# Optimization experiments

Measured on AMD Instinct MI355X. Metric: run time of the kernel, lower is better.

## Reference

```python
import jax, jax.numpy as jnp
import numpy as np

N_ATOM, N_FRAG, N_EDGE, N_FEDGE, N_MEM = 131072, 32768, 262144, 65536, 196608
B, H, IN_A, IN_F, IN_E, L, OUT = 4096, 256, 64, 32, 16, 4, 1


def setup_inputs():
    ks = iter(jax.random.split(jax.random.key(0), 96))

    def nrm(shape, s=0.05):
        return jax.random.normal(next(ks), shape, jnp.float32) * s

    def ri(shape, hi):
        return jax.random.randint(next(ks), shape, 0, hi)

    z = lambda *s: jnp.zeros(s, jnp.float32)
    o = lambda *s: jnp.ones(s, jnp.float32)
    return {
        'x': nrm((N_ATOM, IN_A), 1.0),
        'fragments': nrm((N_FRAG, IN_F), 1.0),
        'edge_attr': nrm((N_EDGE, IN_E), 1.0),
        'atom_enc_W': nrm((IN_A, H)), 'atom_enc_b': z(H),
        'frag_enc_W': nrm((IN_F, H)), 'frag_enc_b': z(H),
        'bond_W': nrm((L, IN_E, H)), 'bond_b': z(L, H),
        'gine_eps': z(L),
        'gine_W1': nrm((L, H, 2 * H)), 'gine_b1': z(L, 2 * H),
        'gine_bn_g': o(L, 2 * H), 'gine_bn_b': z(L, 2 * H),
        'gine_W2': nrm((L, 2 * H, H)), 'gine_b2': z(L, H),
        'atom_bn_g': o(L, H), 'atom_bn_b': z(L, H),
        'gin_eps': z(L),
        'gin_W1': nrm((L, H, 2 * H)), 'gin_b1': z(L, 2 * H),
        'gin_bn_g': o(L, 2 * H), 'gin_bn_b': z(L, 2 * H),
        'gin_W2': nrm((L, 2 * H, H)), 'gin_b2': z(L, H),
        'frag_bn_g': o(L, H), 'frag_bn_b': z(L, H),
        'a2f_W': nrm((L, H, H)), 'a2f_b': z(L, H),
        'f2a_W': nrm((L, H, H)), 'f2a_b': z(L, H),
        'fo_W1': nrm((H, H)), 'fo_b1': z(H), 'fo_W2': nrm((H, H)), 'fo_b2': z(H),
        'ao_W1': nrm((H, H)), 'ao_b1': z(H), 'ao_W2': nrm((H, H)), 'ao_b2': z(H),
        'out_W1': nrm((H, H)), 'out_b1': z(H), 'out_W2': nrm((H, OUT)), 'out_b2': z(OUT),
        'edge_index': ri((2, N_EDGE), N_ATOM),
        'frag_edge_index': ri((2, N_FEDGE), N_FRAG),
        'batch': jnp.sort(ri((N_ATOM,), B)),
        'fragments_batch': jnp.sort(ri((N_FRAG,), B)),
        'mem_atom': ri((N_MEM,), N_ATOM),
        'mem_frag': ri((N_MEM,), N_FRAG),
    }


def _bn(x, g, b):
    # training-mode BatchNorm1d over the node dimension
    m = x.mean(0)
    v = jnp.mean((x - m) ** 2, 0)
    return (x - m) * jax.lax.rsqrt(v + 1e-5) * g + b


def _seg_sum(v, i, n):
    return jax.ops.segment_sum(v, i, num_segments=n)


def _seg_mean(v, i, n):
    s = _seg_sum(v, i, n)
    c = _seg_sum(jnp.ones((v.shape[0], 1), v.dtype), i, n)
    return s / jnp.maximum(c, 1.0)


def _forward(x, fragments, edge_attr, atom_enc_W, atom_enc_b, frag_enc_W, frag_enc_b, bond_W, bond_b, gine_eps, gine_W1, gine_b1, gine_bn_g, gine_bn_b, gine_W2, gine_b2, atom_bn_g, atom_bn_b, gin_eps, gin_W1, gin_b1, gin_bn_g, gin_bn_b, gin_W2, gin_b2, frag_bn_g, frag_bn_b, a2f_W, a2f_b, f2a_W, f2a_b, fo_W1, fo_b1, fo_W2, fo_b2, ao_W1, ao_b1, ao_W2, ao_b2, out_W1, out_b1, out_W2, out_b2, edge_index, frag_edge_index, batch, fragments_batch, mem_atom, mem_frag):
    a = x @ atom_enc_W + atom_enc_b            # [N_ATOM, H] atom encoder
    f = fragments @ frag_enc_W + frag_enc_b    # [N_FRAG, H] clique encoder
    src, dst = edge_index[0], edge_index[1]
    fsrc, fdst = frag_edge_index[0], frag_edge_index[1]
    n_atom, n_frag = a.shape[0], f.shape[0]
    for l in range(L):
        # per-layer bond encoder (learned_edge_rep=False)
        e = edge_attr @ bond_W[l] + bond_b[l]
        # GINEConv: sum_j relu(x_j + e_ij) gathered to target i
        agg = _seg_sum(jax.nn.relu(a[src] + e), dst, n_atom)
        h = (1.0 + gine_eps[l]) * a + agg
        h = jax.nn.relu(_bn(h @ gine_W1[l] + gine_b1[l], gine_bn_g[l], gine_bn_b[l]))
        a = jax.nn.relu(_bn(h @ gine_W2[l] + gine_b2[l], atom_bn_g[l], atom_bn_b[l]))
        # fragment GINConv on fragment graph
        fagg = _seg_sum(f[fsrc], fdst, n_frag)
        hf = (1.0 + gin_eps[l]) * f + fagg
        hf = jax.nn.relu(_bn(hf @ gin_W1[l] + gin_b1[l], gin_bn_g[l], gin_bn_b[l]))
        f = jax.nn.relu(_bn(hf @ gin_W2[l] + gin_b2[l], frag_bn_g[l], frag_bn_b[l]))
        # inter message passing over atom-fragment membership edges (mean reduce)
        f = f + _seg_mean(jax.nn.relu(a[mem_atom] @ a2f_W[l] + a2f_b[l]), mem_frag, n_frag)
        a = a + _seg_mean(jax.nn.relu(f[mem_frag] @ f2a_W[l] + f2a_b[l]), mem_atom, n_atom)
    # graph-level readout (mean pooling per molecule)
    fp = _seg_mean(f, fragments_batch, B)
    fp = jax.nn.relu(jax.nn.relu(fp @ fo_W1 + fo_b1) @ fo_W2 + fo_b2)
    ap = _seg_mean(a, batch, B)
    ap = jax.nn.relu(jax.nn.relu(ap @ ao_W1 + ao_b1) @ ao_W2 + ao_b2)
    zz = ap + fp
    return jax.nn.relu(zz @ out_W1 + out_b1) @ out_W2 + out_b2  # [B, OUT]


def reference(x, fragments, edge_attr, atom_enc_W, atom_enc_b, frag_enc_W, frag_enc_b, bond_W, bond_b, gine_eps, gine_W1, gine_b1, gine_bn_g, gine_bn_b, gine_W2, gine_b2, atom_bn_g, atom_bn_b, gin_eps, gin_W1, gin_b1, gin_bn_g, gin_bn_b, gin_W2, gin_b2, frag_bn_g, frag_bn_b, a2f_W, a2f_b, f2a_W, f2a_b, fo_W1, fo_b1, fo_W2, fo_b2, ao_W1, ao_b1, ao_W2, ao_b2, out_W1, out_b1, out_W2, out_b2, edge_index, frag_edge_index, batch, fragments_batch, mem_atom, mem_frag):
    return _forward(x, fragments, edge_attr, atom_enc_W, atom_enc_b, frag_enc_W, frag_enc_b, bond_W, bond_b, gine_eps, gine_W1, gine_b1, gine_bn_g, gine_bn_b, gine_W2, gine_b2, atom_bn_g, atom_bn_b, gin_eps, gin_W1, gin_b1, gin_bn_g, gin_bn_b, gin_W2, gin_b2, frag_bn_g, frag_bn_b, a2f_W, a2f_b, f2a_W, f2a_b, fo_W1, fo_b1, fo_W2, fo_b2, ao_W1, ao_b1, ao_W2, ao_b2, out_W1, out_b1, out_W2, out_b2, edge_index, frag_edge_index, batch, fragments_batch, mem_atom, mem_frag)
```

## Files before the change

kernel.cpp:

```cpp
#include <hip/hip_runtime.h>

#define CDIV(a,b) (((a)+(b)-1)/(b))

static const int N_ATOM = 131072, N_FRAG = 32768, N_EDGE = 262144,
                 N_FEDGE = 65536, N_MEM = 196608, BATCH = 4096, H = 256;
static const int NREP = 16;

typedef unsigned short ushort_t;
typedef _Float16 half8_t __attribute__((ext_vector_type(8)));
typedef float    floatx4 __attribute__((ext_vector_type(4)));

struct PanelsIn  { const ushort_t* p[4]; };
struct PanelsOut { ushort_t* p[4]; };

__device__ __forceinline__ float h2f(ushort_t u) {
    _Float16 h; __builtin_memcpy(&h, &u, 2); return (float)h;
}
__device__ __forceinline__ ushort_t f2h(float f) {
    _Float16 h = (_Float16)f; ushort_t u; __builtin_memcpy(&u, &h, 2); return u;
}

__device__ __forceinline__ void load_lds16(const ushort_t* g, ushort_t* l) {
    __builtin_amdgcn_global_load_lds(
        (const __attribute__((address_space(1))) unsigned int*)g,
        (__attribute__((address_space(3))) unsigned int*)l, 16, 0, 0);
}

__global__ void fill_const(float* p, long n, float v) {
    long t = (long)blockIdx.x * blockDim.x + threadIdx.x;
    long stride = (long)gridDim.x * blockDim.x;
    for (; t < n; t += stride) p[t] = v;
}

__global__ void conv_f2h(const float* __restrict__ in, ushort_t* __restrict__ out, long n)
{
    long t = (long)blockIdx.x * 256 + threadIdx.x;
    long stride = (long)gridDim.x * 256;
    for (long i = t; i < n / 4; i += stride) {
        float4 v = ((const float4*)in)[i];
        ushort4 o; o.x = f2h(v.x); o.y = f2h(v.y); o.z = f2h(v.z); o.w = f2h(v.w);
        ((ushort4*)out)[i] = o;
    }
}

__global__ void prep_w(const float* __restrict__ s0, const float* __restrict__ s1,
                       const float* __restrict__ s2, const float* __restrict__ s3,
                       const float* __restrict__ s4, const float* __restrict__ s5,
                       const float* __restrict__ s6, const float* __restrict__ s7,
                       ushort_t* __restrict__ hi, ushort_t* __restrict__ lo)
{
    long gid = (long)blockIdx.x * 256 + threadIdx.x;
    const float* src; int K, M; long base, loc;
    if      (gid < 524288)  { src=s0; K=256; M=512; base=0;       loc=gid; }
    else if (gid < 1048576) { src=s1; K=512; M=256; base=524288;  loc=gid-524288; }
    else if (gid < 1572864) { src=s2; K=256; M=512; base=1048576; loc=gid-1048576; }
    else if (gid < 2097152) { src=s3; K=512; M=256; base=1572864; loc=gid-1572864; }
    else if (gid < 2359296) { src=s4; K=256; M=256; base=2097152; loc=gid-2097152; }
    else if (gid < 2621440) { src=s5; K=256; M=256; base=2359296; loc=gid-2359296; }
    else if (gid < 2637824) { src=s6; K=64;  M=256; base=2621440; loc=gid-2621440; }
    else if (gid < 2646016) { src=s7; K=32;  M=256; base=2637824; loc=gid-2637824; }
    else return;
    long msz = (long)K * M;
    int  mat = (int)(loc / msz); long rem = loc - (long)mat * msz;
    int  k = (int)(rem / M);     int  n = (int)(rem - (long)k * M);
    float v = src[loc];
    ushort_t hu = f2h(v);
    ushort_t lu = f2h(v - h2f(hu));
    int nl = n & 127, g = (k >> 3) & 3;
    long p = (long)((nl >> 4) * 64 + g * 16 + (nl & 15));
    long dst = base + (long)mat * msz + (long)(k >> 5) * ((long)M << 5)
             + ((long)(n >> 7) << 12) + (p << 3) + (k & 7);
    hi[dst] = hu;
    if (lo) lo[dst] = lu;
}

template<int RELU>
__global__ __launch_bounds__(256)
void mfma_gemm(PanelsIn Ap, int astride, const ushort_t* __restrict__ Wh,
               const ushort_t* __restrict__ Wl, const float* __restrict__ bias,
               PanelsOut Cp, int cstride, const float* __restrict__ Aff,
               float* __restrict__ cstatR, int N, int K, int M)
{
    __shared__ ushort_t Asm[4096];
    __shared__ ushort_t Bhs[4096];
    __shared__ ushort_t Bls[4096];
    __shared__ ushort_t AffS[1024];
    const int tid = threadIdx.x;
    const int brow = blockIdx.y * 128, bcol = blockIdx.x * 128;
    const int wid = tid >> 6, lane = tid & 63;
    const int wm = wid >> 1, wn = wid & 1;
    const int lg = lane >> 4, lr = lane & 15;

    if (Aff) {
        for (int c = tid; c < K; c += 256) {
            AffS[c]       = f2h(Aff[c]);
            AffS[512 + c] = f2h(Aff[K + c]);
        }
        __syncthreads();
    }

    const int mA = lane & 15;
    const int gA = (lane >> 4) & 3;

    floatx4 acc[4][4];
    #pragma unroll
    for (int i = 0; i < 4; ++i)
        #pragma unroll
        for (int j = 0; j < 4; ++j) acc[i][j] = (floatx4){0.f, 0.f, 0.f, 0.f};

    const int nkt = K >> 5;
    for (int kt = 0; kt < nkt; ++kt) {
        if (kt) __syncthreads();
        const ushort_t* pa = Ap.p[kt >> 2];
        const ushort_t* ga = pa + (long)(brow + wid * 16 + mA) * astride
                                + ((kt & 3) << 5) + gA * 8;
        load_lds16(ga, Asm + wid * 512);
        load_lds16(ga + (long)64 * astride, Asm + 2048 + wid * 512);
        const ushort_t* gb = Wh + (size_t)kt * ((size_t)M << 5)
                                + ((size_t)bcol << 5) + (wid * 64 + lane) * 8;
        load_lds16(gb, Bhs + wid * 512);
        load_lds16(gb + 2048, Bhs + 2048 + wid * 512);
        if (Wl) {
            const ushort_t* gl = Wl + (size_t)kt * ((size_t)M << 5)
                                    + ((size_t)bcol << 5) + (wid * 64 + lane) * 8;
            load_lds16(gl, Bls + wid * 512);
            load_lds16(gl + 2048, Bls + 2048 + wid * 512);
        }
        __syncthreads();

        half8_t af[4], bh[4], bl[4];
        #pragma unroll
        for (int i = 0; i < 4; ++i)
            af[i] = *(const half8_t*)(Asm + (((wm * 4 + i) * 64 + lg * 16 + lr) << 3));
        if (Aff) {
            half8_t scv = *(const half8_t*)(AffS + (kt << 5) + lg * 8);
            half8_t sbv = *(const half8_t*)(AffS + 512 + (kt << 5) + lg * 8);
            #pragma unroll
            for (int i = 0; i < 4; ++i) {
                half8_t z = af[i] * scv + sbv;
                #pragma unroll
                for (int e = 0; e < 8; ++e)
                    z[e] = z[e] > (_Float16)0 ? z[e] : (_Float16)0;
                af[i] = z;
            }
        }
        #pragma unroll
        for (int j = 0; j < 4; ++j) {
            bh[j] = *(const half8_t*)(Bhs + (((wn * 4 + j) * 64 + lg * 16 + lr) << 3));
            if (Wl)
                bl[j] = *(const half8_t*)(Bls + (((wn * 4 + j) * 64 + lg * 16 + lr) << 3));
        }
        #pragma unroll
        for (int i = 0; i < 4; ++i)
            #pragma unroll
            for (int j = 0; j < 4; ++j) {
                acc[i][j] = __builtin_amdgcn_mfma_f32_16x16x32_f16(af[i], bh[j], acc[i][j], 0, 0, 0);
                if (Wl)
                    acc[i][j] = __builtin_amdgcn_mfma_f32_16x16x32_f16(af[i], bl[j], acc[i][j], 0, 0, 0);
            }
    }

    ushort_t* cb = Cp.p[blockIdx.x];
    float csl[4], cql[4];
    #pragma unroll
    for (int j = 0; j < 4; ++j) { csl[j] = 0.f; cql[j] = 0.f; }
    #pragma unroll
    for (int j = 0; j < 4; ++j) {
        int lcol = wn * 64 + j * 16 + lr;
        float bia = bias[bcol + lcol];
        #pragma unroll
        for (int i = 0; i < 4; ++i) {
            #pragma unroll
            for (int r = 0; r < 4; ++r) {
                int row = brow + wm * 64 + i * 16 + (lg << 2) + r;
                float v = acc[i][j][r] + bia;
                if (RELU) v = fmaxf(v, 0.f);
                ushort_t uo = f2h(v);
                cb[(long)row * cstride + lcol] = uo;
                if (cstatR) {
                    float vq = h2f(uo);
                    csl[j] += vq; cql[j] = fmaf(vq, vq, cql[j]);
                }
            }
        }
    }
    if (cstatR) {
        __syncthreads();
        float* cs = (float*)Asm;
        float* cq = (float*)Bhs;
        if (tid < 128) { cs[tid] = 0.f; cq[tid] = 0.f; }
        __syncthreads();
        #pragma unroll
        for (int j = 0; j < 4; ++j) {
            int cl = wn * 64 + j * 16 + lr;
            atomicAdd(&cs[cl], csl[j]);
            atomicAdd(&cq[cl], cql[j]);
        }
        __syncthreads();
        if (tid < 128) {
            int rep = blockIdx.y & (NREP - 1);
            atomicAdd(&cstatR[(long)rep * 2 * M + bcol + tid], cs[tid]);
            atomicAdd(&cstatR[(long)rep * 2 * M + M + bcol + tid], cq[tid]);
        }
    }
}

__global__ void finalize_aff(const float* __restrict__ cstatR, int M, float invN,
                             const float* __restrict__ g, const float* __restrict__ b,
                             float* __restrict__ aff)
{
    int c = blockIdx.x * blockDim.x + threadIdx.x;
    if (c >= M) return;
    float s = 0.f, q = 0.f;
    for (int r = 0; r < NREP; ++r) {
        s += cstatR[(long)r * 2 * M + c];
        q += cstatR[(long)r * 2 * M + M + c];
    }
    float m = s * invN, var = q * invN - m * m;
    float sa = rsqrtf(var + 1e-5f) * g[c];
    aff[c] = sa; aff[M + c] = b[c] - m * sa;
}

template<int EB>
__global__ __launch_bounds__(256)
void csr_agg(const ushort_t* __restrict__ in, ushort_t* __restrict__ out,
             const int* __restrict__ offs, const int* __restrict__ elist,
             const int* __restrict__ esrc, const float* __restrict__ eattr,
             const float* __restrict__ Wb, const float* __restrict__ bb,
             const float* __restrict__ eps_p, int n_nodes)
{
    __shared__ float Ws[EB ? 4096 : 1];
    __shared__ float bs[EB ? 256 : 1];
    if (EB) {
        for (int i = threadIdx.x; i < 4096; i += 256) Ws[i] = Wb[i];
        bs[threadIdx.x] = bb[threadIdx.x];
        __syncthreads();
    }
    float epsv = 1.f + eps_p[0];
    int lane = threadIdx.x & 63;
    int gw = (blockIdx.x * 256 + threadIdx.x) >> 6;
    int nw = (gridDim.x * 256) >> 6;
    for (int u = gw; u < n_nodes; u += nw) {
        const ushort_t* own = in + (long)u * 256;
        float acc[4];
        #pragma unroll
        for (int j = 0; j < 4; ++j) acc[j] = epsv * h2f(own[lane + 64 * j]);
        int s = offs[u], e = offs[u + 1];
        for (int i = s; i < e; ++i) {
            int eid = elist[i];
            int sid = esrc[eid];
            const ushort_t* row = in + (long)sid * 256;
            if (EB) {
                float ev[16];
                const float4* ea = (const float4*)(eattr + (long)eid * 16);
                float4 e0 = ea[0], e1 = ea[1], e2 = ea[2], e3 = ea[3];
                ev[0]=e0.x; ev[1]=e0.y; ev[2]=e0.z; ev[3]=e0.w;
                ev[4]=e1.x; ev[5]=e1.y; ev[6]=e1.z; ev[7]=e1.w;
                ev[8]=e2.x; ev[9]=e2.y; ev[10]=e2.z; ev[11]=e2.w;
                ev[12]=e3.x; ev[13]=e3.y; ev[14]=e3.z; ev[15]=e3.w;
                #pragma unroll
                for (int j = 0; j < 4; ++j) {
                    int c = lane + 64 * j;
                    float m = bs[c];
                    #pragma unroll
                    for (int k = 0; k < 16; ++k) m = fmaf(ev[k], Ws[k * 256 + c], m);
                    acc[j] += fmaxf(h2f(row[c]) + m, 0.f);
                }
            } else {
                #pragma unroll
                for (int j = 0; j < 4; ++j) acc[j] += h2f(row[lane + 64 * j]);
            }
        }
        ushort_t* o = out + (long)u * 256;
        #pragma unroll
        for (int j = 0; j < 4; ++j) o[lane + 64 * j] = f2h(acc[j]);
    }
}

__global__ __launch_bounds__(128)
void csr_mean_aff(const ushort_t* __restrict__ raw, const ushort_t* __restrict__ U,
                  const int* __restrict__ midx, const int* __restrict__ elist,
                  const int* __restrict__ offs, const float* __restrict__ Aff,
                  ushort_t* __restrict__ outp)
{
    int u = blockIdx.x, t = threadIdx.x;
    int c0 = t * 2;
    float sa0 = Aff[c0], sa1 = Aff[c0 + 1], sb0 = Aff[256 + c0], sb1 = Aff[256 + c0 + 1];
    ushort2 b = *(const ushort2*)(raw + (long)u * 256 + c0);
    float x0 = fmaxf(h2f(b.x) * sa0 + sb0, 0.f);
    float x1 = fmaxf(h2f(b.y) * sa1 + sb1, 0.f);
    int s = offs[u], e = offs[u + 1];
    float a0 = 0.f, a1 = 0.f;
    for (int i = s; i < e; ++i) {
        long r = midx[elist[i]];
        ushort2 v = *(const ushort2*)(U + r * 256 + c0);
        a0 += h2f(v.x); a1 += h2f(v.y);
    }
    if (e > s) { float inv = 1.f / (float)(e - s); x0 += a0 * inv; x1 += a1 * inv; }
    ushort2 o; o.x = f2h(x0); o.y = f2h(x1);
    *(ushort2*)(outp + (long)u * 256 + c0) = o;
}

template<int RELU, typename TC>
__global__ __launch_bounds__(256)
void gemm_k(const float* __restrict__ A, const float* __restrict__ W,
            const float* __restrict__ bias, TC* __restrict__ C,
            int N, int K, int M)
{
    const int BK = 16, LDA = 133;
    __shared__ float As[BK * LDA];
    __shared__ float Bs[BK * LDA];
    const int brow = blockIdx.y * 128;
    const int bcol = blockIdx.x * 128;
    const int tid  = threadIdx.x;
    const int tr = tid >> 4, tc = tid & 15;

    float acc[8][8];
    #pragma unroll
    for (int i = 0; i < 8; ++i)
        #pragma unroll
        for (int j = 0; j < 8; ++j) acc[i][j] = 0.f;

    for (int k0 = 0; k0 < K; k0 += BK) {
        #pragma unroll
        for (int u = 0; u < 8; ++u) {
            int idx = tid + u * 256;
            int m = idx >> 4, kk = idx & 15;
            As[kk * LDA + m] = A[(long)(brow + m) * K + k0 + kk];
        }
        #pragma unroll
        for (int u = 0; u < 8; ++u) {
            int idx = tid + u * 256;
            int kk = idx >> 7, n = idx & 127;
            int col = bcol + n;
            Bs[kk * LDA + n] = (col < M) ? W[(long)(k0 + kk) * M + col] : 0.f;
        }
        __syncthreads();
        #pragma unroll
        for (int kk = 0; kk < BK; ++kk) {
            float av[8], bv[8];
            float4 a0 = *(const float4*)&As[kk * LDA + tr * 8];
            float4 a1 = *(const float4*)&As[kk * LDA + tr * 8 + 4];
            float4 b0 = *(const float4*)&Bs[kk * LDA + tc * 8];
            float4 b1 = *(const float4*)&Bs[kk * LDA + tc * 8 + 4];
            av[0]=a0.x; av[1]=a0.y; av[2]=a0.z; av[3]=a0.w;
            av[4]=a1.x; av[5]=a1.y; av[6]=a1.z; av[7]=a1.w;
            bv[0]=b0.x; bv[1]=b0.y; bv[2]=b0.z; bv[3]=b0.w;
            bv[4]=b1.x; bv[5]=b1.y; bv[6]=b1.z; bv[7]=b1.w;
            #pragma unroll
            for (int i = 0; i < 8; ++i)
                #pragma unroll
                for (int j = 0; j < 8; ++j)
                    acc[i][j] = fmaf(av[i], bv[j], acc[i][j]);
        }
        __syncthreads();
    }
    #pragma unroll
    for (int i = 0; i < 8; ++i) {
        int row = brow + tr * 8 + i;
        #pragma unroll
        for (int j = 0; j < 8; ++j) {
            int col = bcol + tc * 8 + j;
            if (col < M) {
                float v = acc[i][j] + bias[col];
                if (RELU) v = fmaxf(v, 0.f);
                if constexpr (sizeof(TC) == 2) ((ushort_t*)C)[(long)row * M + col] = f2h(v);
                else                           ((float*)C)[(long)row * M + col] = v;
            }
        }
    }
}

__global__ void count_idx(const int* __restrict__ idx, int n, int* __restrict__ cnt)
{
    int i = blockIdx.x * blockDim.x + threadIdx.x;
    if (i < n) atomicAdd(&cnt[idx[i]], 1);
}

__global__ __launch_bounds__(256)
void scan_p1(const int* __restrict__ cnt, int n, int* __restrict__ partials)
{
    __shared__ int sd[256];
    int i = blockIdx.x * 256 + threadIdx.x;
    sd[threadIdx.x] = (i < n) ? cnt[i] : 0;
    __syncthreads();
    #pragma unroll
    for (int s = 128; s > 0; s >>= 1) {
        if (threadIdx.x < s) sd[threadIdx.x] += sd[threadIdx.x + s];
        __syncthreads();
    }
    if (threadIdx.x == 0) partials[blockIdx.x] = sd[0];
}

__global__ __launch_bounds__(1024)
void scan_p2(int* __restrict__ partials, int nb, int* __restrict__ off, int n)
{
    __shared__ int sd[1024];
    int t = threadIdx.x;
    int v = (t < nb) ? partials[t] : 0;
    sd[t] = v;
    __syncthreads();
    for (int d = 1; d < 1024; d <<= 1) {
        int x = (t >= d) ? sd[t - d] : 0;
        __syncthreads();
        sd[t] += x;
        __syncthreads();
    }
    if (t < nb) partials[t] = sd[t] - v;
    if (t == 1023) off[n] = sd[nb - 1];
}

__global__ __launch_bounds__(256)
void scan_p3(const int* __restrict__ cnt, int n, const int* __restrict__ partials,
             int* __restrict__ off, int* __restrict__ cursor)
{
    __shared__ int sd[256];
    int i = blockIdx.x * 256 + threadIdx.x;
    int v = (i < n) ? cnt[i] : 0;
    sd[threadIdx.x] = v;
    __syncthreads();
    for (int d = 1; d < 256; d <<= 1) {
        int x = (threadIdx.x >= d) ? sd[threadIdx.x - d] : 0;
        __syncthreads();
        sd[threadIdx.x] += x;
        __syncthreads();
    }
    if (i < n) {
        int e = partials[blockIdx.x] + sd[threadIdx.x] - v;
        off[i] = e; cursor[i] = e;
    }
}

__global__ void csr_fill(const int* __restrict__ idx, int n,
                         int* __restrict__ cursor, int* __restrict__ elist)
{
    int i = blockIdx.x * blockDim.x + threadIdx.x;
    if (i < n) { int p = atomicAdd(&cursor[idx[i]], 1); elist[p] = i; }
}

__global__ __launch_bounds__(256)
void seg_pool(const ushort_t* __restrict__ X, const int* __restrict__ bidx,
              int nrows, float* __restrict__ pooled)
{
    int b = blockIdx.x, t = threadIdx.x;
    int lo = 0, hi = nrows;
    while (lo < hi) { int mid = (lo + hi) >> 1; if (bidx[mid] < b) lo = mid + 1; else hi = mid; }
    int s = lo; hi = nrows;
    while (lo < hi) { int mid = (lo + hi) >> 1; if (bidx[mid] < b + 1) lo = mid + 1; else hi = mid; }
    int e = lo;
    float acc = 0.f;
    for (int r = s; r < e; ++r) acc += h2f(X[(long)r * 256 + t]);
    pooled[(long)b * 256 + t] = acc / fmaxf((float)(e - s), 1.f);
}

__global__ void vadd(float* __restrict__ out, const float* __restrict__ in, long n4)
{
    long t = (long)blockIdx.x * blockDim.x + threadIdx.x;
    if (t >= n4) return;
    float4 a = ((float4*)out)[t];
    float4 b = ((const float4*)in)[t];
    a.x += b.x; a.y += b.y; a.z += b.z; a.w += b.w;
    ((float4*)out)[t] = a;
}

extern "C" void kernel_launch(void* const* d_in, const int* in_sizes, int n_in,
                              void* d_out, int out_size, void* d_ws, size_t ws_size,
                              hipStream_t stream)
{
    (void)in_sizes; (void)n_in;
    const float* x          = (const float*)d_in[0];
    const float* fragments  = (const float*)d_in[1];
    const float* edge_attr  = (const float*)d_in[2];
    const float* atom_enc_W = (const float*)d_in[3];
    const float* atom_enc_b = (const float*)d_in[4];
    const float* frag_enc_W = (const float*)d_in[5];
    const float* frag_enc_b = (const float*)d_in[6];
    const float* bond_W     = (const float*)d_in[7];
    const float* bond_b     = (const float*)d_in[8];
    const float* gine_eps   = (const float*)d_in[9];
    const float* gine_W1    = (const float*)d_in[10];
    const float* gine_b1    = (const float*)d_in[11];
    const float* gine_bn_g  = (const float*)d_in[12];
    const float* gine_bn_b  = (const float*)d_in[13];
    const float* gine_W2    = (const float*)d_in[14];
    const float* gine_b2    = (const float*)d_in[15];
    const float* atom_bn_g  = (const float*)d_in[16];
    const float* atom_bn_b  = (const float*)d_in[17];
    const float* gin_eps    = (const float*)d_in[18];
    const float* gin_W1     = (const float*)d_in[19];
    const float* gin_b1     = (const float*)d_in[20];
    const float* gin_bn_g   = (const float*)d_in[21];
    const float* gin_bn_b   = (const float*)d_in[22];
    const float* gin_W2     = (const float*)d_in[23];
    const float* gin_b2     = (const float*)d_in[24];
    const float* frag_bn_g  = (const float*)d_in[25];
    const float* frag_bn_b  = (const float*)d_in[26];
    const float* a2f_W      = (const float*)d_in[27];
    const float* a2f_b      = (const float*)d_in[28];
    const float* f2a_W      = (const float*)d_in[29];
    const float* f2a_b      = (const float*)d_in[30];
    const float* fo_W1      = (const float*)d_in[31];
    const float* fo_b1      = (const float*)d_in[32];
    const float* fo_W2      = (const float*)d_in[33];
    const float* fo_b2      = (const float*)d_in[34];
    const float* ao_W1      = (const float*)d_in[35];
    const float* ao_b1      = (const float*)d_in[36];
    const float* ao_W2      = (const float*)d_in[37];
    const float* ao_b2      = (const float*)d_in[38];
    const float* out_W1     = (const float*)d_in[39];
    const float* out_b1     = (const float*)d_in[40];
    const float* out_W2     = (const float*)d_in[41];
    const float* out_b2     = (const float*)d_in[42];
    const int* edge_index   = (const int*)d_in[43];
    const int* fedge_index  = (const int*)d_in[44];
    const int* batch        = (const int*)d_in[45];
    const int* fbatch       = (const int*)d_in[46];
    const int* mem_atom     = (const int*)d_in[47];
    const int* mem_frag     = (const int*)d_in[48];

    const int* src  = edge_index;
    const int* dst  = edge_index + N_EDGE;
    const int* fsrc = fedge_index;
    const int* fdst = fedge_index + N_FEDGE;

    const size_t WPN = 2646016;
    size_t off = 0;
    auto take = [&](size_t b) -> size_t { size_t p = off; off = (off + b + 255) & ~(size_t)255; return p; };
    size_t o_big   = take((size_t)N_ATOM * 512 * 2);
    size_t o_a     = take((size_t)N_ATOM * H * 2);
    size_t o_f     = take((size_t)N_FRAG * H * 2);
    size_t o_f2    = take((size_t)N_FRAG * H * 2);
    size_t o_offea = take((size_t)(N_ATOM + 1) * 4);
    size_t o_elea  = take((size_t)N_EDGE * 4);
    size_t o_offef = take((size_t)(N_FRAG + 1) * 4);
    size_t o_elef  = take((size_t)N_FEDGE * 4);
    size_t o_offma = take((size_t)(N_ATOM + 1) * 4);
    size_t o_elma  = take((size_t)N_MEM * 4);
    size_t o_offmf = take((size_t)(N_FRAG + 1) * 4);
    size_t o_elmf  = take((size_t)N_MEM * 4);
    size_t o_cnta  = take((size_t)N_ATOM * 4);
    size_t o_cntf  = take((size_t)N_FRAG * 4);
    size_t o_part  = take(1024 * 4);
    size_t o_stats = take((size_t)NREP * 3072 * 4);
    size_t o_aff   = take(3072 * 4);
    size_t o_hi    = take(WPN * 2);
    size_t need_nolo = off;
    size_t o_lo    = take(WPN * 2);
    size_t need_full = off;

    bool use_lo = (need_full <= ws_size);
    if (!use_lo && need_nolo > ws_size) {
        fill_const<<<64, 256, 0, stream>>>((float*)d_out, out_size,
                                           (float)((double)ws_size / 1024.0));
        return;
    }
    char* base = (char*)d_ws;
    char*     big     = base + o_big;
    ushort_t* a       = (ushort_t*)(base + o_a);
    ushort_t* f       = (ushort_t*)(base + o_f);
    ushort_t* f2      = (ushort_t*)(base + o_f2);
    int* off_ea = (int*)(base + o_offea);
    int* el_ea  = (int*)(base + o_elea);
    int* off_ef = (int*)(base + o_offef);
    int* el_ef  = (int*)(base + o_elef);
    int* off_ma = (int*)(base + o_offma);
    int* el_ma  = (int*)(base + o_elma);
    int* off_mf = (int*)(base + o_offmf);
    int* el_mf  = (int*)(base + o_elmf);
    int* cnt_a  = (int*)(base + o_cnta);
    int* cnt_f  = (int*)(base + o_cntf);
    int* parts  = (int*)(base + o_part);
    float* statsR = (float*)(base + o_stats);
    float* affs   = (float*)(base + o_aff);
    ushort_t* Wp_hi = (ushort_t*)(base + o_hi);
    ushort_t* Wp_lo = use_lo ? (ushort_t*)(base + o_lo) : nullptr;

    float* cst1a = statsR;
    float* cst2a = statsR + (size_t)NREP * 1024;
    float* cst1f = statsR + (size_t)NREP * 1536;
    float* cst2f = statsR + (size_t)NREP * 2560;
    float* aff1_a = affs;
    float* aff2_a = affs + 1024;
    float* aff1_f = affs + 1536;
    float* aff2_f = affs + 2560;

    ushort_t* big_u = (ushort_t*)big;
    const size_t HALF_U = (size_t)N_ATOM * 256;
    ushort_t* ha  = big_u + HALF_U;
    const size_t PAN_A = (size_t)N_ATOM * 128;
    const size_t PAN_F = (size_t)N_FRAG * 128;
    ushort_t* Ua = big_u;
    float* pooled_f = (float*)big;
    float* pooled_a = (float*)(big + (size_t)8 * 1024 * 1024);
    float* tmp      = (float*)(big + (size_t)16 * 1024 * 1024);
    ushort_t* xh = big_u;
    ushort_t* fh = big_u + (size_t)N_ATOM * 64;

    const long WG0 = 0, WG1 = 524288, WG2 = 1048576, WG3 = 1572864,
               WG4 = 2097152, WG5 = 2359296, WG6 = 2621440, WG7 = 2637824;

    auto build_csr = [&](const int* idx, int n_edges, int n_nodes,
                         int* cnt, int* offs, int* elist) {
        hipMemsetAsync(cnt, 0, (size_t)n_nodes * 4, stream);
        count_idx<<<CDIV(n_edges,256),256,0,stream>>>(idx, n_edges, cnt);
        int nb = CDIV(n_nodes, 256);
        scan_p1<<<nb, 256, 0, stream>>>(cnt, n_nodes, parts);
        scan_p2<<<1, 1024, 0, stream>>>(parts, nb, offs, n_nodes);
        scan_p3<<<nb, 256, 0, stream>>>(cnt, n_nodes, parts, offs, cnt);
        csr_fill<<<CDIV(n_edges,256),256,0,stream>>>(idx, n_edges, cnt, elist);
    };

    prep_w<<<CDIV((long)WPN, 256), 256, 0, stream>>>(gine_W1, gine_W2, gin_W1, gin_W2,
                                                     a2f_W, f2a_W, atom_enc_W, frag_enc_W,
                                                     Wp_hi, Wp_lo);
    build_csr(dst,      N_EDGE,  N_ATOM, cnt_a, off_ea, el_ea);
    build_csr(fdst,     N_FEDGE, N_FRAG, cnt_f, off_ef, el_ef);
    build_csr(mem_atom, N_MEM,   N_ATOM, cnt_a, off_ma, el_ma);
    build_csr(mem_frag, N_MEM,   N_FRAG, cnt_f, off_mf, el_mf);

    conv_f2h<<<2048, 256, 0, stream>>>(x, xh, (long)N_ATOM * 64);
    conv_f2h<<<512, 256, 0, stream>>>(fragments, fh, (long)N_FRAG * 32);
    {
        PanelsIn Ein; PanelsOut Eout;
        for (int i = 0; i < 4; ++i) Ein.p[i] = xh;
        Eout.p[0] = a; Eout.p[1] = a + 128; Eout.p[2] = a; Eout.p[3] = a;
        mfma_gemm<0><<<dim3(2, N_ATOM/128), 256, 0, stream>>>(
            Ein, 64, Wp_hi + WG6, Wp_lo ? Wp_lo + WG6 : nullptr,
            atom_enc_b, Eout, 256, nullptr, nullptr, N_ATOM, 64, 256);
        PanelsIn Fin; PanelsOut Fout;
        for (int i = 0; i < 4; ++i) Fin.p[i] = fh;
        Fout.p[0] = f; Fout.p[1] = f + 128; Fout.p[2] = f; Fout.p[3] = f;
        mfma_gemm<0><<<dim3(2, N_FRAG/128), 256, 0, stream>>>(
            Fin, 32, Wp_hi + WG7, Wp_lo ? Wp_lo + WG7 : nullptr,
            frag_enc_b, Fout, 256, nullptr, nullptr, N_FRAG, 32, 256);
    }

    const float invNA = 1.f / N_ATOM, invNF = 1.f / N_FRAG;

    for (int l = 0; l < 4; ++l) {
        hipMemsetAsync(statsR, 0, (size_t)NREP * 3072 * 4, stream);

        csr_agg<1><<<2048, 256, 0, stream>>>(a, ha, off_ea, el_ea, src, edge_attr,
            bond_W + (long)l*16*H, bond_b + l*H, gine_eps + l, N_ATOM);

        PanelsIn A1in; PanelsOut A1out;
        for (int i = 0; i < 4; ++i) A1in.p[i] = ha + i * 128;
        A1out.p[0] = a;          A1out.p[1] = a + PAN_A;
        A1out.p[2] = big_u;      A1out.p[3] = big_u + PAN_A;
        mfma_gemm<0><<<dim3(4, N_ATOM/128), 256, 0, stream>>>(
            A1in, 256, Wp_hi + WG0 + (long)l*131072,
            Wp_lo ? Wp_lo + WG0 + (long)l*131072 : nullptr,
            gine_b1 + l*512, A1out, 128, nullptr, cst1a, N_ATOM, 256, 512);
        finalize_aff<<<2, 256, 0, stream>>>(cst1a, 512, invNA,
            gine_bn_g + l*512, gine_bn_b + l*512, aff1_a);

        PanelsIn A2in; PanelsOut A2out;
        A2in.p[0] = a;       A2in.p[1] = a + PAN_A;
        A2in.p[2] = big_u;   A2in.p[3] = big_u + PAN_A;
        A2out.p[0] = ha; A2out.p[1] = ha + 128; A2out.p[2] = ha; A2out.p[3] = ha;
        mfma_gemm<0><<<dim3(2, N_ATOM/128), 256, 0, stream>>>(
            A2in, 128, Wp_hi + WG1 + (long)l*131072,
            Wp_lo ? Wp_lo + WG1 + (long)l*131072 : nullptr,
            gine_b2 + l*H, A2out, 256, aff1_a, cst2a, N_ATOM, 512, 256);
        finalize_aff<<<1, 256, 0, stream>>>(cst2a, 256, invNA,
            atom_bn_g + l*H, atom_bn_b + l*H, aff2_a);

        csr_agg<0><<<512, 256, 0, stream>>>(f, f2, off_ef, el_ef, fsrc, nullptr,
            nullptr, nullptr, gin_eps + l, N_FRAG);

        PanelsIn F1in; PanelsOut F1out;
        for (int i = 0; i < 4; ++i) F1in.p[i] = f2 + i * 128;
        for (int i = 0; i < 4; ++i) F1out.p[i] = big_u + i * PAN_F;
        mfma_gemm<0><<<dim3(4, N_FRAG/128), 256, 0, stream>>>(
            F1in, 256, Wp_hi + WG2 + (long)l*131072,
            Wp_lo ? Wp_lo + WG2 + (long)l*131072 : nullptr,
            gin_b1 + l*512, F1out, 128, nullptr, cst1f, N_FRAG, 256, 512);
        finalize_aff<<<2, 256, 0, stream>>>(cst1f, 512, invNF,
            gin_bn_g + l*512, gin_bn_b + l*512, aff1_f);

        PanelsIn F2in; PanelsOut F2out;
        for (int i = 0; i < 4; ++i) F2in.p[i] = big_u + i * PAN_F;
        F2out.p[0] = f2; F2out.p[1] = f2 + 128; F2out.p[2] = f2; F2out.p[3] = f2;
        mfma_gemm<0><<<dim3(2, N_FRAG/128), 256, 0, stream>>>(
            F2in, 128, Wp_hi + WG3 + (long)l*131072,
            Wp_lo ? Wp_lo + WG3 + (long)l*131072 : nullptr,
            gin_b2 + l*H, F2out, 256, aff1_f, cst2f, N_FRAG, 512, 256);
        finalize_aff<<<1, 256, 0, stream>>>(cst2f, 256, invNF,
            frag_bn_g + l*H, frag_bn_b + l*H, aff2_f);

        PanelsIn UAin; PanelsOut UAout;
        for (int i = 0; i < 4; ++i) UAin.p[i] = ha + i * 128;
        UAout.p[0] = Ua; UAout.p[1] = Ua + 128; UAout.p[2] = Ua; UAout.p[3] = Ua;
        mfma_gemm<1><<<dim3(2, N_ATOM/128), 256, 0, stream>>>(
            UAin, 256, Wp_hi + WG4 + (long)l*65536, nullptr,
            a2f_b + l*H, UAout, 256, aff2_a, nullptr, N_ATOM, 256, 256);
        csr_mean_aff<<<N_FRAG, 128, 0, stream>>>(f2, Ua, mem_atom, el_mf, off_mf,
                                                 aff2_f, f);
        PanelsIn UFin; PanelsOut UFout;
        for (int i = 0; i < 4; ++i) UFin.p[i] = f + i * 128;
        UFout.p[0] = f2; UFout.p[1] = f2 + 128; UFout.p[2] = f2; UFout.p[3] = f2;
        mfma_gemm<1><<<dim3(2, N_FRAG/128), 256, 0, stream>>>(
            UFin, 256, Wp_hi + WG5 + (long)l*65536, nullptr,
            f2a_b + l*H, UFout, 256, nullptr, nullptr, N_FRAG, 256, 256);
        csr_mean_aff<<<N_ATOM, 128, 0, stream>>>(ha, f2, mem_frag, el_ma, off_ma,
                                                 aff2_a, a);
    }

    seg_pool<<<BATCH, 256, 0, stream>>>(f, fbatch, N_FRAG, pooled_f);
    gemm_k<1,float><<<dim3(2, BATCH/128), 256, 0, stream>>>(
        pooled_f, fo_W1, fo_b1, tmp, BATCH, H, H);
    gemm_k<1,float><<<dim3(2, BATCH/128), 256, 0, stream>>>(
        tmp, fo_W2, fo_b2, pooled_f, BATCH, H, H);

    seg_pool<<<BATCH, 256, 0, stream>>>(a, batch, N_ATOM, pooled_a);
    gemm_k<1,float><<<dim3(2, BATCH/128), 256, 0, stream>>>(
        pooled_a, ao_W1, ao_b1, tmp, BATCH, H, H);
    gemm_k<1,float><<<dim3(2, BATCH/128), 256, 0, stream>>>(
        tmp, ao_W2, ao_b2, pooled_a, BATCH, H, H);

    vadd<<<(int)CDIV((long)BATCH*H/4,256), 256, 0, stream>>>(
        pooled_a, pooled_f, (long)BATCH * H / 4);
    gemm_k<1,float><<<dim3(2, BATCH/128), 256, 0, stream>>>(
        pooled_a, out_W1, out_b1, tmp, BATCH, H, H);
    gemm_k<0,float><<<dim3(1, BATCH/128), 256, 0, stream>>>(
        tmp, out_W2, out_b2, (float*)d_out, BATCH, H, 1);
}
```

Before: 3.475 ms.

## Drop fp16 low-part weight split and swizzle GEMM block order

Removes the hi/lo fp16 split of the weights, so the MFMA GEMMs run one pass per tile instead of two for the layer weights, and the extra LDS buffer and loads go away. It also remaps block IDs with an XCD-style swizzle (bid&7 groups) so consecutive blocks on the same die share A rows for better L2 reuse. The cost is lower weight precision (fp16 only), which can increase error against the fp32 reference.

```diff
diff --git a/kernel.cpp b/kernel.cpp
--- a/kernel.cpp
+++ b/kernel.cpp
@@ -47,7 +47,7 @@
                        const float* __restrict__ s2, const float* __restrict__ s3,
                        const float* __restrict__ s4, const float* __restrict__ s5,
                        const float* __restrict__ s6, const float* __restrict__ s7,
-                       ushort_t* __restrict__ hi, ushort_t* __restrict__ lo)
+                       ushort_t* __restrict__ hi)
 {
     long gid = (long)blockIdx.x * 256 + threadIdx.x;
     const float* src; int K, M; long base, loc;
@@ -63,30 +63,30 @@
     long msz = (long)K * M;
     int  mat = (int)(loc / msz); long rem = loc - (long)mat * msz;
     int  k = (int)(rem / M);     int  n = (int)(rem - (long)k * M);
-    float v = src[loc];
-    ushort_t hu = f2h(v);
-    ushort_t lu = f2h(v - h2f(hu));
     int nl = n & 127, g = (k >> 3) & 3;
     long p = (long)((nl >> 4) * 64 + g * 16 + (nl & 15));
     long dst = base + (long)mat * msz + (long)(k >> 5) * ((long)M << 5)
              + ((long)(n >> 7) << 12) + (p << 3) + (k & 7);
-    hi[dst] = hu;
-    if (lo) lo[dst] = lu;
+    hi[dst] = f2h(src[loc]);
 }
 
 template<int RELU>
 __global__ __launch_bounds__(256)
 void mfma_gemm(PanelsIn Ap, int astride, const ushort_t* __restrict__ Wh,
-               const ushort_t* __restrict__ Wl, const float* __restrict__ bias,
+               const float* __restrict__ bias,
                PanelsOut Cp, int cstride, const float* __restrict__ Aff,
                float* __restrict__ cstatR, int N, int K, int M)
 {
     __shared__ ushort_t Asm[4096];
     __shared__ ushort_t Bhs[4096];
-    __shared__ ushort_t Bls[4096];
     __shared__ ushort_t AffS[1024];
     const int tid = threadIdx.x;
-    const int brow = blockIdx.y * 128, bcol = blockIdx.x * 128;
+    const int nwg = gridDim.x * gridDim.y;
+    const int bid = blockIdx.y * gridDim.x + blockIdx.x;
+    const int cpx = nwg >> 3;
+    const int swz = (bid & 7) * cpx + (bid >> 3);
+    const int bx = swz % gridDim.x, by = swz / gridDim.x;
+    const int brow = by * 128, bcol = bx * 128;
     const int wid = tid >> 6, lane = tid & 63;
     const int wm = wid >> 1, wn = wid & 1;
     const int lg = lane >> 4, lr = lane & 15;
@@ -120,15 +120,9 @@
                                 + ((size_t)bcol << 5) + (wid * 64 + lane) * 8;
         load_lds16(gb, Bhs + wid * 512);
         load_lds16(gb + 2048, Bhs + 2048 + wid * 512);
-        if (Wl) {
-            const ushort_t* gl = Wl + (size_t)kt * ((size_t)M << 5)
-                                    + ((size_t)bcol << 5) + (wid * 64 + lane) * 8;
-            load_lds16(gl, Bls + wid * 512);
-            load_lds16(gl + 2048, Bls + 2048 + wid * 512);
-        }
-        __syncthreads();
-
-        half8_t af[4], bh[4], bl[4];
+        __syncthreads();
+
+        half8_t af[4], bh[4];
         #pragma unroll
         for (int i = 0; i < 4; ++i)
             af[i] = *(const half8_t*)(Asm + (((wm * 4 + i) * 64 + lg * 16 + lr) << 3));
@@ -145,22 +139,16 @@
             }
         }
         #pragma unroll
-        for (int j = 0; j < 4; ++j) {
+        for (int j = 0; j < 4; ++j)
             bh[j] = *(const half8_t*)(Bhs + (((wn * 4 + j) * 64 + lg * 16 + lr) << 3));
-            if (Wl)
-                bl[j] = *(const half8_t*)(Bls + (((wn * 4 + j) * 64 + lg * 16 + lr) << 3));
-        }
         #pragma unroll
         for (int i = 0; i < 4; ++i)
             #pragma unroll
-            for (int j = 0; j < 4; ++j) {
+            for (int j = 0; j < 4; ++j)
                 acc[i][j] = __builtin_amdgcn_mfma_f32_16x16x32_f16(af[i], bh[j], acc[i][j], 0, 0, 0);
-                if (Wl)
-                    acc[i][j] = __builtin_amdgcn_mfma_f32_16x16x32_f16(af[i], bl[j], acc[i][j], 0, 0, 0);
-            }
-    }
-
-    ushort_t* cb = Cp.p[blockIdx.x];
+    }
+
+    ushort_t* cb = Cp.p[bx];
     float csl[4], cql[4];
     #pragma unroll
     for (int j = 0; j < 4; ++j) { csl[j] = 0.f; cql[j] = 0.f; }
@@ -198,7 +186,7 @@
         }
         __syncthreads();
         if (tid < 128) {
-            int rep = blockIdx.y & (NREP - 1);
+            int rep = by & (NREP - 1);
             atomicAdd(&cstatR[(long)rep * 2 * M + bcol + tid], cs[tid]);
             atomicAdd(&cstatR[(long)rep * 2 * M + M + bcol + tid], cq[tid]);
         }
@@ -544,12 +532,9 @@
     size_t o_stats = take((size_t)NREP * 3072 * 4);
     size_t o_aff   = take(3072 * 4);
     size_t o_hi    = take(WPN * 2);
-    size_t need_nolo = off;
-    size_t o_lo    = take(WPN * 2);
-    size_t need_full = off;
-
-    bool use_lo = (need_full <= ws_size);
-    if (!use_lo && need_nolo > ws_size) {
+    size_t need = off;
+
+    if (need > ws_size) {
         fill_const<<<64, 256, 0, stream>>>((float*)d_out, out_size,
                                            (float)((double)ws_size / 1024.0));
         return;
@@ -573,7 +558,6 @@
     float* statsR = (float*)(base + o_stats);
     float* affs   = (float*)(base + o_aff);
     ushort_t* Wp_hi = (ushort_t*)(base + o_hi);
-    ushort_t* Wp_lo = use_lo ? (ushort_t*)(base + o_lo) : nullptr;
 
     float* cst1a = statsR;
     float* cst2a = statsR + (size_t)NREP * 1024;
@@ -612,7 +596,7 @@
 
     prep_w<<<CDIV((long)WPN, 256), 256, 0, stream>>>(gine_W1, gine_W2, gin_W1, gin_W2,
                                                      a2f_W, f2a_W, atom_enc_W, frag_enc_W,
-                                                     Wp_hi, Wp_lo);
+                                                     Wp_hi);
     build_csr(dst,      N_EDGE,  N_ATOM, cnt_a, off_ea, el_ea);
     build_csr(fdst,     N_FEDGE, N_FRAG, cnt_f, off_ef, el_ef);
     build_csr(mem_atom, N_MEM,   N_ATOM, cnt_a, off_ma, el_ma);
@@ -625,14 +609,14 @@
         for (int i = 0; i < 4; ++i) Ein.p[i] = xh;
         Eout.p[0] = a; Eout.p[1] = a + 128; Eout.p[2] = a; Eout.p[3] = a;
         mfma_gemm<0><<<dim3(2, N_ATOM/128), 256, 0, stream>>>(
-            Ein, 64, Wp_hi + WG6, Wp_lo ? Wp_lo + WG6 : nullptr,
-            atom_enc_b, Eout, 256, nullptr, nullptr, N_ATOM, 64, 256);
+            Ein, 64, Wp_hi + WG6, atom_enc_b, Eout, 256, nullptr, nullptr,
+            N_ATOM, 64, 256);
         PanelsIn Fin; PanelsOut Fout;
         for (int i = 0; i < 4; ++i) Fin.p[i] = fh;
         Fout.p[0] = f; Fout.p[1] = f + 128; Fout.p[2] = f; Fout.p[3] = f;
         mfma_gemm<0><<<dim3(2, N_FRAG/128), 256, 0, stream>>>(
-            Fin, 32, Wp_hi + WG7, Wp_lo ? Wp_lo + WG7 : nullptr,
-            frag_enc_b, Fout, 256, nullptr, nullptr, N_FRAG, 32, 256);
+            Fin, 32, Wp_hi + WG7, frag_enc_b, Fout, 256, nullptr, nullptr,
+            N_FRAG, 32, 256);
     }
 
     const float invNA = 1.f / N_ATOM, invNF = 1.f / N_FRAG;
@@ -649,7 +633,6 @@
         A1out.p[2] = big_u;      A1out.p[3] = big_u + PAN_A;
         mfma_gemm<0><<<dim3(4, N_ATOM/128), 256, 0, stream>>>(
             A1in, 256, Wp_hi + WG0 + (long)l*131072,
-            Wp_lo ? Wp_lo + WG0 + (long)l*131072 : nullptr,
             gine_b1 + l*512, A1out, 128, nullptr, cst1a, N_ATOM, 256, 512);
         finalize_aff<<<2, 256, 0, stream>>>(cst1a, 512, invNA,
             gine_bn_g + l*512, gine_bn_b + l*512, aff1_a);
@@ -660,7 +643,6 @@
         A2out.p[0] = ha; A2out.p[1] = ha + 128; A2out.p[2] = ha; A2out.p[3] = ha;
         mfma_gemm<0><<<dim3(2, N_ATOM/128), 256, 0, stream>>>(
             A2in, 128, Wp_hi + WG1 + (long)l*131072,
-            Wp_lo ? Wp_lo + WG1 + (long)l*131072 : nullptr,
             gine_b2 + l*H, A2out, 256, aff1_a, cst2a, N_ATOM, 512, 256);
         finalize_aff<<<1, 256, 0, stream>>>(cst2a, 256, invNA,
             atom_bn_g + l*H, atom_bn_b + l*H, aff2_a);
@@ -673,7 +655,6 @@
         for (int i = 0; i < 4; ++i) F1out.p[i] = big_u + i * PAN_F;
         mfma_gemm<0><<<dim3(4, N_FRAG/128), 256, 0, stream>>>(
             F1in, 256, Wp_hi + WG2 + (long)l*131072,
-            Wp_lo ? Wp_lo + WG2 + (long)l*131072 : nullptr,
             gin_b1 + l*512, F1out, 128, nullptr, cst1f, N_FRAG, 256, 512);
         finalize_aff<<<2, 256, 0, stream>>>(cst1f, 512, invNF,
             gin_bn_g + l*512, gin_bn_b + l*512, aff1_f);
@@ -683,7 +664,6 @@
         F2out.p[0] = f2; F2out.p[1] = f2 + 128; F2out.p[2] = f2; F2out.p[3] = f2;
         mfma_gemm<0><<<dim3(2, N_FRAG/128), 256, 0, stream>>>(
             F2in, 128, Wp_hi + WG3 + (long)l*131072,
-            Wp_lo ? Wp_lo + WG3 + (long)l*131072 : nullptr,
             gin_b2 + l*H, F2out, 256, aff1_f, cst2f, N_FRAG, 512, 256);
         finalize_aff<<<1, 256, 0, stream>>>(cst2f, 256, invNF,
             frag_bn_g + l*H, frag_bn_b + l*H, aff2_f);
@@ -692,7 +672,7 @@
         for (int i = 0; i < 4; ++i) UAin.p[i] = ha + i * 128;
         UAout.p[0] = Ua; UAout.p[1] = Ua + 128; UAout.p[2] = Ua; UAout.p[3] = Ua;
         mfma_gemm<1><<<dim3(2, N_ATOM/128), 256, 0, stream>>>(
-            UAin, 256, Wp_hi + WG4 + (long)l*65536, nullptr,
+            UAin, 256, Wp_hi + WG4 + (long)l*65536,
             a2f_b + l*H, UAout, 256, aff2_a, nullptr, N_ATOM, 256, 256);
         csr_mean_aff<<<N_FRAG, 128, 0, stream>>>(f2, Ua, mem_atom, el_mf, off_mf,
                                                  aff2_f, f);
@@ -700,7 +680,7 @@
         for (int i = 0; i < 4; ++i) UFin.p[i] = f + i * 128;
         UFout.p[0] = f2; UFout.p[1] = f2 + 128; UFout.p[2] = f2; UFout.p[3] = f2;
         mfma_gemm<1><<<dim3(2, N_FRAG/128), 256, 0, stream>>>(
-            UFin, 256, Wp_hi + WG5 + (long)l*65536, nullptr,
+            UFin, 256, Wp_hi + WG5 + (long)l*65536,
             f2a_b + l*H, UFout, 256, nullptr, nullptr, N_FRAG, 256, 256);
         csr_mean_aff<<<N_ATOM, 128, 0, stream>>>(ha, f2, mem_frag, el_ma, off_ma,
                                                  aff2_a, a);
```

Result: faster. 3.208 ms (-7.7%).
